# Performance work log

Hardware: AMD Instinct MI355X
Metric: run time of the kernel (lower is better)

The kernel has to match this reference:

```python
import math
import jax, jax.numpy as jnp
import numpy as np

HEADS = 16


def setup_inputs() -> dict:
    key = jax.random.key(0)
    k1, k2, k3, k4, k5 = jax.random.split(key, 5)
    B, S, D = 2, 2048, 1024
    return {
        "x": jax.random.normal(k1, (B, S, D), dtype=jnp.float32),
        "Wqkv": jax.random.normal(k2, (3 * D, D), dtype=jnp.float32) * (1.0 / math.sqrt(D)),
        "bqkv": jax.random.normal(k3, (3 * D,), dtype=jnp.float32) * 0.02,
        "Wo": jax.random.normal(k4, (D, D), dtype=jnp.float32) * (1.0 / math.sqrt(D)),
        "bo": jax.random.normal(k5, (D,), dtype=jnp.float32) * 0.02,
    }


def reference(x, Wqkv, bqkv, Wo, bo):
    B, S, D = x.shape
    H = HEADS
    hd = D // H  # head dim
    qkv = x @ Wqkv.T + bqkv                      # (B, S, 3D)
    # Faithful to torch: direct contiguous reshape (NOT a transpose-based head split)
    qkv = qkv.reshape(B, H, S, 3 * hd)           # (B, H, S, 3*hd)
    q, k, v = jnp.split(qkv, 3, axis=-1)         # each (B, H, S, hd)
    scores = jnp.einsum("bhsd,bhtd->bhst", q, k) * (1.0 / math.sqrt(hd))
    attn = jax.nn.softmax(scores, axis=-1)       # (B, H, S, S)
    vals = jnp.einsum("bhst,bhtd->bhsd", attn, v)
    vals = vals.reshape(B, S, D)                 # faithful direct reshape back
    return vals @ Wo.T + bo
```

## Files before the change

### kernel.cpp

```cpp
#include <hip/hip_runtime.h>
#include <stdint.h>

typedef unsigned short u16;
typedef __attribute__((ext_vector_type(8))) short short8;
typedef __attribute__((ext_vector_type(4))) float f32x4;
typedef __attribute__((ext_vector_type(16))) float f32x16;
typedef __attribute__((ext_vector_type(8))) __bf16 bf16x8;
typedef __attribute__((ext_vector_type(4))) unsigned u32x4;

#define DEV static __device__ __forceinline__

template <typename T>
DEV auto mfma_try(T a, T b, f32x4 c, int)
    -> decltype(__builtin_amdgcn_mfma_f32_16x16x32_bf16(a, b, c, 0, 0, 0)) {
  return __builtin_amdgcn_mfma_f32_16x16x32_bf16(a, b, c, 0, 0, 0);
}
template <typename T>
DEV f32x4 mfma_try(T a, T b, f32x4 c, long) {
  return __builtin_amdgcn_mfma_f32_16x16x32_bf16(
      __builtin_bit_cast(bf16x8, a), __builtin_bit_cast(bf16x8, b), c, 0, 0, 0);
}
DEV f32x4 MFMA(short8 a, short8 b, f32x4 c) { return mfma_try(a, b, c, 0); }

template <typename T>
DEV auto mfma32_try(T a, T b, f32x16 c, int)
    -> decltype(__builtin_amdgcn_mfma_f32_32x32x16_bf16(a, b, c, 0, 0, 0)) {
  return __builtin_amdgcn_mfma_f32_32x32x16_bf16(a, b, c, 0, 0, 0);
}
template <typename T>
DEV f32x16 mfma32_try(T a, T b, f32x16 c, long) {
  return __builtin_amdgcn_mfma_f32_32x32x16_bf16(
      __builtin_bit_cast(bf16x8, a), __builtin_bit_cast(bf16x8, b), c, 0, 0, 0);
}
DEV f32x16 MFMA32(short8 a, short8 b, f32x16 c) { return mfma32_try(a, b, c, 0); }

DEV void gload16(const u16* g, u16* lds) {
  __builtin_amdgcn_global_load_lds((unsigned int*)g, (unsigned int*)lds, 16, 0, 0);
}

DEV u16 f2bf(float f) {
  unsigned u = __float_as_uint(f);
  u = (u + 0x7FFFu + ((u >> 16) & 1u)) >> 16;
  return (u16)u;
}

DEV float exp2fast(float x) {
  float r;
  asm("v_exp_f32 %0, %1" : "=v"(r) : "v"(x));
  return r;
}

DEV unsigned cvtpk_bf16(float lo, float hi_) {
  unsigned r;
  asm("v_cvt_pk_bf16_f32 %0, %1, %2" : "=v"(r) : "v"(lo), "v"(hi_));
  return r;
}

DEV void permswap(unsigned& a, unsigned& b) {
  asm volatile("v_permlane32_swap_b32 %0, %1" : "+v"(a), "+v"(b));
}

__global__ void cvt_kernel(const float* __restrict__ x, const float* __restrict__ wq,
                           const float* __restrict__ wo, u16* __restrict__ xb,
                           u16* __restrict__ wqb, u16* __restrict__ wob) {
  const int N1 = 4194304 / 4, N2 = 3145728 / 4, N3 = 1048576 / 4;
  const int total = N1 + N2 + N3;
  for (int i = blockIdx.x * blockDim.x + threadIdx.x; i < total;
       i += gridDim.x * blockDim.x) {
    const float4* s;
    u16* d;
    int off;
    if (i < N1) { s = (const float4*)x; d = xb; off = i; }
    else if (i < N1 + N2) { s = (const float4*)wq; d = wqb; off = i - N1; }
    else { s = (const float4*)wo; d = wob; off = i - N1 - N2; }
    float4 v = s[off];
    ushort4 o;
    o.x = f2bf(v.x); o.y = f2bf(v.y); o.z = f2bf(v.z); o.w = f2bf(v.w);
    ((ushort4*)d)[off] = o;
  }
}

__global__ __launch_bounds__(256, 4) void gemm1_128(
    const u16* __restrict__ A, const u16* __restrict__ Bm,
    const float* __restrict__ bias,
    u16* __restrict__ Qb, u16* __restrict__ Kb, u16* __restrict__ Vb) {
  __shared__ u16 SM[128 * 136];
  const int K = 1024;
  const int tid = threadIdx.x;
  const int lane = tid & 63;
  const int wave = tid >> 6;
  const int wr = wave >> 1, wc = wave & 1;
  const int l15 = lane & 15, l4 = lane >> 4;
  const int m0 = blockIdx.y * 128, n0 = blockIdx.x * 128;

  f32x4 acc[4][4] = {};

  const u16* ga = A + (size_t)(m0 + (tid >> 2)) * K + (tid & 3) * 8;
  const u16* gb = Bm + (size_t)(n0 + (tid >> 2)) * K + (tid & 3) * 8;
  const size_t rstep = (size_t)64 * K;

  auto stage = [&](int buf, int kt) {
    u16* la = SM + buf * 8192 + tid * 8;
    u16* lb = la + 4096;
    gload16(ga + kt, la);
    gload16(ga + kt + rstep, la + 2048);
    gload16(gb + kt, lb);
    gload16(gb + kt + rstep, lb + 2048);
  };

  stage(0, 0);
  for (int t = 0; t < 32; ++t) {
    const int cur = t & 1;
    if (t + 1 < 32) {
      stage(cur ^ 1, (t + 1) * 32);
      asm volatile("s_waitcnt vmcnt(4)" ::: "memory");
    } else {
      asm volatile("s_waitcnt vmcnt(0)" ::: "memory");
    }
    __builtin_amdgcn_s_barrier();

    const u16* As = SM + cur * 8192;
    const u16* Bs = As + 4096;
    short8 af[4], bfr[4];
#pragma unroll
    for (int i = 0; i < 4; ++i)
      af[i] = *(const short8*)(As + (wr * 64 + i * 16 + l15) * 32 + l4 * 8);
#pragma unroll
    for (int i = 0; i < 4; ++i)
      bfr[i] = *(const short8*)(Bs + (wc * 64 + i * 16 + l15) * 32 + l4 * 8);
    __builtin_amdgcn_s_setprio(1);
#pragma unroll
    for (int i = 0; i < 4; ++i)
#pragma unroll
      for (int j = 0; j < 4; ++j) acc[i][j] = MFMA(af[i], bfr[j], acc[i][j]);
    __builtin_amdgcn_s_setprio(0);
    __builtin_amdgcn_s_barrier();
  }

#pragma unroll
  for (int nj = 0; nj < 4; ++nj) {
    const int cl = wc * 64 + nj * 16 + l15;
    const float bv = bias[n0 + cl];
#pragma unroll
    for (int mi = 0; mi < 4; ++mi)
#pragma unroll
      for (int r = 0; r < 4; ++r) {
        const int ml = wr * 64 + mi * 16 + l4 * 4 + r;
        SM[ml * 136 + cl] = f2bf(acc[mi][nj][r] + bv);
      }
  }
  __syncthreads();

  const int ml = tid >> 1;
  const int h = tid & 1;
  const int m = m0 + ml;
  const int c0 = n0 + h * 64;
  const int chunk = c0 / 192;
  const int sel = (c0 - chunk * 192) >> 6;
  u16* const dst = (sel == 0) ? Qb : ((sel == 1) ? Kb : Vb);
  const int s = m & 2047;
  const int bh = (m >> 11) * 16 + (s >> 7);
  const int s2 = (s & 127) * 16 + chunk;
  u16* const drow = dst + ((size_t)bh * 2048 + s2) * 64;
  const u16* const srow = SM + ml * 136 + h * 64;
#pragma unroll
  for (int g = 0; g < 8; ++g)
    *(short8*)(drow + g * 8) = *(const short8*)(srow + g * 8);
}

__global__ __launch_bounds__(256, 4) void gemm2_64(
    const u16* __restrict__ A, const u16* __restrict__ Bm,
    const float* __restrict__ bias, float* __restrict__ Cf) {
  __shared__ u16 SM2[2 * 6144];
  const int K = 1024, N = 1024;
  const int tid = threadIdx.x;
  const int lane = tid & 63;
  const int wave = tid >> 6;
  const int l15 = lane & 15, l4 = lane >> 4;
  const int m0 = blockIdx.y * 64, n0 = blockIdx.x * 128;

  f32x4 acc[4][2] = {};

  const u16* ga = A + (size_t)(m0 + (tid >> 2)) * K + (tid & 3) * 8;
  const u16* gb = Bm + (size_t)(n0 + (tid >> 2)) * K + (tid & 3) * 8;
  const size_t rstep = (size_t)64 * K;

  auto stage = [&](int buf, int kt) {
    u16* la = SM2 + buf * 6144 + tid * 8;
    u16* lb = SM2 + buf * 6144 + 2048 + tid * 8;
    gload16(ga + kt, la);
    gload16(gb + kt, lb);
    gload16(gb + kt + rstep, lb + 2048);
  };

  stage(0, 0);
  for (int t = 0; t < 32; ++t) {
    const int cur = t & 1;
    if (t + 1 < 32) {
      stage(cur ^ 1, (t + 1) * 32);
      asm volatile("s_waitcnt vmcnt(3)" ::: "memory");
    } else {
      asm volatile("s_waitcnt vmcnt(0)" ::: "memory");
    }
    __builtin_amdgcn_s_barrier();

    const u16* As = SM2 + cur * 6144;
    const u16* Bs = As + 2048;
    short8 af[4], bfr[2];
#pragma unroll
    for (int i = 0; i < 4; ++i)
      af[i] = *(const short8*)(As + (i * 16 + l15) * 32 + l4 * 8);
#pragma unroll
    for (int j = 0; j < 2; ++j)
      bfr[j] = *(const short8*)(Bs + (wave * 32 + j * 16 + l15) * 32 + l4 * 8);
    __builtin_amdgcn_s_setprio(1);
#pragma unroll
    for (int i = 0; i < 4; ++i)
#pragma unroll
      for (int j = 0; j < 2; ++j) acc[i][j] = MFMA(af[i], bfr[j], acc[i][j]);
    __builtin_amdgcn_s_setprio(0);
    __builtin_amdgcn_s_barrier();
  }

#pragma unroll
  for (int nj = 0; nj < 2; ++nj) {
    const int c = n0 + wave * 32 + nj * 16 + l15;
    const float bv = bias[c];
#pragma unroll
    for (int mi = 0; mi < 4; ++mi)
#pragma unroll
      for (int r = 0; r < 4; ++r) {
        const int m = m0 + mi * 16 + l4 * 4 + r;
        Cf[(size_t)m * N + c] = acc[mi][nj][r] + bv;
      }
  }
}

__global__ __launch_bounds__(256) void vtrans_kernel(const u16* __restrict__ Vn,
                                                     u16* __restrict__ VT) {
  __shared__ u16 T[64 * 72];
  const int tid = threadIdx.x;
  const int bh = blockIdx.x >> 5;
  const int s0 = (blockIdx.x & 31) * 64;
  const int r = tid >> 3, c8 = tid & 7;
#pragma unroll
  for (int i = 0; i < 2; ++i) {
    const int s = r + i * 32;
    short8 v = *(const short8*)(Vn + ((size_t)bh * 2048 + s0 + s) * 64 + c8 * 8);
#pragma unroll
    for (int j = 0; j < 8; ++j) T[(c8 * 8 + j) * 72 + s] = (u16)v[j];
  }
  __syncthreads();
#pragma unroll
  for (int i = 0; i < 2; ++i) {
    const int d = (tid >> 3) + i * 32;
    short8 v = *(const short8*)(&T[d * 72 + (tid & 7) * 8]);
    *(short8*)(VT + ((size_t)bh * 64 + d) * 2048 + s0 + (tid & 7) * 8) = v;
  }
}

__global__ __launch_bounds__(512) void attn_kernel(
    const u16* __restrict__ Qg, const u16* __restrict__ Kg,
    const u16* __restrict__ VTg, u16* __restrict__ v2) {
  __shared__ __align__(16) char smem[65536];
  u16* const KS = (u16*)smem;
  u16* const VS = (u16*)smem + 16384;
  float* const FM = (float*)smem;

  const int tid = threadIdx.x;
  const int lane = tid & 63;
  const int half = tid >> 8;
  const int tid256 = tid & 255;
  const int w4 = (tid >> 6) & 3;
  const int l31 = lane & 31;
  const int hi = lane >> 5;

  const int bid = blockIdx.x;
  const int logical = (bid & 7) * 64 + (bid >> 3);
  const int bh = logical >> 4;
  const int qt = logical & 15;

  const u16* Qh = Qg + (size_t)bh * 2048 * 64;
  const u16* Kh = Kg + (size_t)bh * 2048 * 64;
  const u16* VTh = VTg + (size_t)bh * 64 * 2048;

  const int q0 = qt * 128 + w4 * 32;
  const float C1 = 0.18033688f;

  short8 qf[4];
#pragma unroll
  for (int d_ = 0; d_ < 4; ++d_)
    qf[d_] = *(const short8*)(Qh + (size_t)(q0 + l31) * 64 + d_ * 16 + hi * 8);

  f32x16 ot[2] = {};
  float ls4[4] = {0.f, 0.f, 0.f, 0.f};

  const int r8 = tid256 >> 3;
  const int c16 = tid256 & 7;
  const int xr = l31 & 7;
  const int Tbase = half * 16;

  auto stage = [&](int buf, int T) {
    u16* kd = KS + (half * 2 + buf) * 4096 + tid256 * 8;
    u16* vd = VS + (half * 2 + buf) * 4096 + tid256 * 8;
#pragma unroll
    for (int i = 0; i < 2; ++i) {
      const int row = i * 32 + r8;
      gload16(Kh + (size_t)(T * 64 + row) * 64 + ((c16 ^ (row & 7)) * 8),
              kd + i * 2048);
    }
#pragma unroll
    for (int i = 0; i < 2; ++i) {
      const int d = i * 32 + r8;
      gload16(VTh + (size_t)d * 2048 + T * 64 + ((c16 ^ (d & 7)) * 8),
              vd + i * 2048);
    }
  };

  stage(0, Tbase);
  __syncthreads();

  for (int t = 0; t < 16; ++t) {
    const int cur = t & 1;
    if (t + 1 < 16) stage(cur ^ 1, Tbase + t + 1);

    const u16* Kb = KS + (half * 2 + cur) * 4096;
    const u16* Vb = VS + (half * 2 + cur) * 4096;

    f32x16 st[2] = {};
    __builtin_amdgcn_s_setprio(1);
#pragma unroll
    for (int n = 0; n < 2; ++n)
#pragma unroll
      for (int d_ = 0; d_ < 4; ++d_) {
        short8 kf = *(const short8*)(Kb + (n * 32 + l31) * 64 +
                                     (((d_ * 2 + hi) ^ xr) * 8));
        st[n] = MFMA32(kf, qf[d_], st[n]);
      }
    __builtin_amdgcn_s_setprio(0);

#pragma unroll
    for (int r = 0; r < 16; ++r) {
      st[0][r] = exp2fast(st[0][r] * C1);
      st[1][r] = exp2fast(st[1][r] * C1);
    }
#pragma unroll
    for (int i = 0; i < 4; ++i)
      ls4[i] += ((st[0][i] + st[0][i + 4]) + (st[0][i + 8] + st[0][i + 12])) +
                ((st[1][i] + st[1][i + 4]) + (st[1][i + 8] + st[1][i + 12]));

    short8 pf[2][2];
#pragma unroll
    for (int n = 0; n < 2; ++n) {
      unsigned W[4][2];
#pragma unroll
      for (int j = 0; j < 4; ++j)
#pragma unroll
        for (int pp = 0; pp < 2; ++pp)
          W[j][pp] = cvtpk_bf16(st[n][4 * j + 2 * pp], st[n][4 * j + 2 * pp + 1]);
#pragma unroll
      for (int ks = 0; ks < 2; ++ks) {
        unsigned x0 = W[2 * ks][0], y0 = W[2 * ks + 1][0];
        unsigned x1 = W[2 * ks][1], y1 = W[2 * ks + 1][1];
        permswap(x0, y0);
        permswap(x1, y1);
        u32x4 pw = {x0, x1, y0, y1};
        pf[n][ks] = __builtin_bit_cast(short8, pw);
      }
    }

    __builtin_amdgcn_s_setprio(1);
#pragma unroll
    for (int db = 0; db < 2; ++db)
#pragma unroll
      for (int ksg = 0; ksg < 4; ++ksg) {
        short8 vf = *(const short8*)(Vb + (db * 32 + l31) * 64 +
                                     (((ksg * 2 + hi) ^ xr) * 8));
        ot[db] = MFMA32(vf, pf[ksg >> 1][ksg & 1], ot[db]);
      }
    __builtin_amdgcn_s_setprio(0);

    __syncthreads();
  }

  float l = (ls4[0] + ls4[1]) + (ls4[2] + ls4[3]);
  l += __shfl_xor(l, 32);

  if (half == 1) {
    float* F = FM + (size_t)(w4 * 64 + lane) * 33;
#pragma unroll
    for (int r = 0; r < 16; ++r) {
      F[r] = ot[0][r];
      F[16 + r] = ot[1][r];
    }
    F[32] = l;
  }
  __syncthreads();
  if (half == 0) {
    const float* F = FM + (size_t)(w4 * 64 + lane) * 33;
    const float inv = 1.0f / (l + F[32]);

    const int s2v = q0 + l31;
    const int rowO = (bh >> 4) * 2048 + (bh & 15) * 128 + (s2v >> 4);
    const int colb = (s2v & 15) * 64;
#pragma unroll
    for (int db = 0; db < 2; ++db)
#pragma unroll
      for (int g = 0; g < 4; ++g) {
        ushort4 w;
        w.x = f2bf((ot[db][4 * g + 0] + F[db * 16 + 4 * g + 0]) * inv);
        w.y = f2bf((ot[db][4 * g + 1] + F[db * 16 + 4 * g + 1]) * inv);
        w.z = f2bf((ot[db][4 * g + 2] + F[db * 16 + 4 * g + 2]) * inv);
        w.w = f2bf((ot[db][4 * g + 3] + F[db * 16 + 4 * g + 3]) * inv);
        const int d = db * 32 + 8 * g + 4 * hi;
        *(ushort4*)(v2 + (size_t)rowO * 1024 + colb + d) = w;
      }
  }
}

extern "C" void kernel_launch(void* const* d_in, const int* in_sizes, int n_in,
                              void* d_out, int out_size, void* d_ws, size_t ws_size,
                              hipStream_t stream) {
  const float* x = (const float*)d_in[0];
  const float* Wqkv = (const float*)d_in[1];
  const float* bqkv = (const float*)d_in[2];
  const float* Wo = (const float*)d_in[3];
  const float* bo = (const float*)d_in[4];
  float* out = (float*)d_out;

  char* ws = (char*)d_ws;
  u16* xb   = (u16*)(ws);
  u16* wqb  = (u16*)(ws + 8388608);
  u16* wob  = (u16*)(ws + 14680064);
  u16* Qb   = (u16*)(ws + 16777216);
  u16* Kb   = (u16*)(ws + 25165824);
  u16* VTb  = (u16*)(ws + 33554432);
  u16* v2   = (u16*)(ws + 41943040);
  u16* Vnat = v2;

  cvt_kernel<<<2048, 256, 0, stream>>>(x, Wqkv, Wo, xb, wqb, wob);

  dim3 g1(24, 32);
  gemm1_128<<<g1, 256, 0, stream>>>(xb, wqb, bqkv, Qb, Kb, Vnat);

  vtrans_kernel<<<1024, 256, 0, stream>>>(Vnat, VTb);

  attn_kernel<<<512, 512, 0, stream>>>(Qb, Kb, VTb, v2);

  dim3 g2(8, 64);
  gemm2_64<<<g2, 256, 0, stream>>>(v2, wob, bo, out);
}
```

Before: 114.6 us.

## Triple-buffer QKV GEMM loads and give each attention wave two query tiles

The QKV projection GEMM moves from double to triple buffering in shared memory, keeping two K-tiles in flight, and drops the occupancy hint in its launch bounds. The attention kernel shrinks from 512 to 256 threads per block. Each wave now handles 64 query rows (two 32-row subtiles), so every K and V fragment read from LDS feeds two MFMAs. This aims to cut LDS traffic per MFMA and hide global load latency better, at the cost of more registers per wave and fewer waves per block to hide latency.

Result: slower. 130.4 us (+13.8%).

```diff
diff --git a/kernel.cpp b/kernel.cpp
--- a/kernel.cpp
+++ b/kernel.cpp
@@ -80,11 +80,11 @@
   }
 }
 
-__global__ __launch_bounds__(256, 4) void gemm1_128(
+__global__ __launch_bounds__(256) void gemm1_128(
     const u16* __restrict__ A, const u16* __restrict__ Bm,
     const float* __restrict__ bias,
     u16* __restrict__ Qb, u16* __restrict__ Kb, u16* __restrict__ Vb) {
-  __shared__ u16 SM[128 * 136];
+  __shared__ u16 SM[3 * 8192];
   const int K = 1024;
   const int tid = threadIdx.x;
   const int lane = tid & 63;
@@ -109,10 +109,13 @@
   };
 
   stage(0, 0);
+  stage(1, 32);
   for (int t = 0; t < 32; ++t) {
-    const int cur = t & 1;
-    if (t + 1 < 32) {
-      stage(cur ^ 1, (t + 1) * 32);
+    const int cur = t % 3;
+    if (t + 2 < 32) {
+      stage((t + 2) % 3, (t + 2) * 32);
+      asm volatile("s_waitcnt vmcnt(8)" ::: "memory");
+    } else if (t + 1 < 32) {
       asm volatile("s_waitcnt vmcnt(4)" ::: "memory");
     } else {
       asm volatile("s_waitcnt vmcnt(0)" ::: "memory");
@@ -259,7 +262,7 @@
   }
 }
 
-__global__ __launch_bounds__(512) void attn_kernel(
+__global__ __launch_bounds__(256) void attn_kernel(
     const u16* __restrict__ Qg, const u16* __restrict__ Kg,
     const u16* __restrict__ VTg, u16* __restrict__ v2) {
   __shared__ __align__(16) char smem[65536];
@@ -269,9 +272,9 @@
 
   const int tid = threadIdx.x;
   const int lane = tid & 63;
-  const int half = tid >> 8;
-  const int tid256 = tid & 255;
-  const int w4 = (tid >> 6) & 3;
+  const int wave = tid >> 6;
+  const int qw = wave & 1;
+  const int half = wave >> 1;
   const int l31 = lane & 31;
   const int hi = lane >> 5;
 
@@ -284,88 +287,96 @@
   const u16* Kh = Kg + (size_t)bh * 2048 * 64;
   const u16* VTh = VTg + (size_t)bh * 64 * 2048;
 
-  const int q0 = qt * 128 + w4 * 32;
+  const int q0 = qt * 128 + qw * 64;
   const float C1 = 0.18033688f;
 
-  short8 qf[4];
-#pragma unroll
-  for (int d_ = 0; d_ < 4; ++d_)
-    qf[d_] = *(const short8*)(Qh + (size_t)(q0 + l31) * 64 + d_ * 16 + hi * 8);
-
-  f32x16 ot[2] = {};
-  float ls4[4] = {0.f, 0.f, 0.f, 0.f};
-
-  const int r8 = tid256 >> 3;
-  const int c16 = tid256 & 7;
+  short8 qf[2][4];
+#pragma unroll
+  for (int qs = 0; qs < 2; ++qs)
+#pragma unroll
+    for (int d_ = 0; d_ < 4; ++d_)
+      qf[qs][d_] = *(const short8*)(Qh + (size_t)(q0 + qs * 32 + l31) * 64 +
+                                    d_ * 16 + hi * 8);
+
+  f32x16 ot[2][2] = {};
+  float ls4[2][4] = {};
+
   const int xr = l31 & 7;
-  const int Tbase = half * 16;
-
-  auto stage = [&](int buf, int T) {
-    u16* kd = KS + (half * 2 + buf) * 4096 + tid256 * 8;
-    u16* vd = VS + (half * 2 + buf) * 4096 + tid256 * 8;
-#pragma unroll
-    for (int i = 0; i < 2; ++i) {
-      const int row = i * 32 + r8;
-      gload16(Kh + (size_t)(T * 64 + row) * 64 + ((c16 ^ (row & 7)) * 8),
-              kd + i * 2048);
-    }
-#pragma unroll
-    for (int i = 0; i < 2; ++i) {
-      const int d = i * 32 + r8;
-      gload16(VTh + (size_t)d * 2048 + T * 64 + ((c16 ^ (d & 7)) * 8),
-              vd + i * 2048);
+
+  auto stage = [&](int buf, int tl) {
+#pragma unroll
+    for (int i = 0; i < 4; ++i) {
+      const int FB = i * 256 + tid;
+      const int hh = FB >> 9;
+      const int b = FB & 511;
+      const int r = b >> 3, cb = b & 7;
+      gload16(Kh + (size_t)(hh * 1024 + tl * 64 + r) * 64 + ((cb ^ (r & 7)) * 8),
+              KS + hh * 8192 + buf * 4096 + b * 8);
+    }
+#pragma unroll
+    for (int i = 0; i < 4; ++i) {
+      const int FB = i * 256 + tid;
+      const int hh = FB >> 9;
+      const int b = FB & 511;
+      const int r = b >> 3, cb = b & 7;
+      gload16(VTh + (size_t)r * 2048 + hh * 1024 + tl * 64 + ((cb ^ (r & 7)) * 8),
+              VS + hh * 8192 + buf * 4096 + b * 8);
     }
   };
 
-  stage(0, Tbase);
+  stage(0, 0);
   __syncthreads();
 
   for (int t = 0; t < 16; ++t) {
     const int cur = t & 1;
-    if (t + 1 < 16) stage(cur ^ 1, Tbase + t + 1);
-
-    const u16* Kb = KS + (half * 2 + cur) * 4096;
-    const u16* Vb = VS + (half * 2 + cur) * 4096;
-
-    f32x16 st[2] = {};
-    __builtin_amdgcn_s_setprio(1);
-#pragma unroll
-    for (int n = 0; n < 2; ++n)
+    if (t + 1 < 16) stage(cur ^ 1, t + 1);
+
+    const u16* Kb = KS + half * 8192 + cur * 4096;
+    const u16* Vb = VS + half * 8192 + cur * 4096;
+
+    short8 pf[2][2][2];
+#pragma unroll
+    for (int n = 0; n < 2; ++n) {
+      f32x16 s0 = {}, s1 = {};
+      __builtin_amdgcn_s_setprio(1);
 #pragma unroll
       for (int d_ = 0; d_ < 4; ++d_) {
         short8 kf = *(const short8*)(Kb + (n * 32 + l31) * 64 +
                                      (((d_ * 2 + hi) ^ xr) * 8));
-        st[n] = MFMA32(kf, qf[d_], st[n]);
-      }
-    __builtin_amdgcn_s_setprio(0);
-
-#pragma unroll
-    for (int r = 0; r < 16; ++r) {
-      st[0][r] = exp2fast(st[0][r] * C1);
-      st[1][r] = exp2fast(st[1][r] * C1);
-    }
-#pragma unroll
-    for (int i = 0; i < 4; ++i)
-      ls4[i] += ((st[0][i] + st[0][i + 4]) + (st[0][i + 8] + st[0][i + 12])) +
-                ((st[1][i] + st[1][i + 4]) + (st[1][i + 8] + st[1][i + 12]));
-
-    short8 pf[2][2];
-#pragma unroll
-    for (int n = 0; n < 2; ++n) {
-      unsigned W[4][2];
-#pragma unroll
-      for (int j = 0; j < 4; ++j)
-#pragma unroll
-        for (int pp = 0; pp < 2; ++pp)
-          W[j][pp] = cvtpk_bf16(st[n][4 * j + 2 * pp], st[n][4 * j + 2 * pp + 1]);
-#pragma unroll
-      for (int ks = 0; ks < 2; ++ks) {
-        unsigned x0 = W[2 * ks][0], y0 = W[2 * ks + 1][0];
-        unsigned x1 = W[2 * ks][1], y1 = W[2 * ks + 1][1];
-        permswap(x0, y0);
-        permswap(x1, y1);
-        u32x4 pw = {x0, x1, y0, y1};
-        pf[n][ks] = __builtin_bit_cast(short8, pw);
+        s0 = MFMA32(kf, qf[0][d_], s0);
+        s1 = MFMA32(kf, qf[1][d_], s1);
+      }
+      __builtin_amdgcn_s_setprio(0);
+
+#pragma unroll
+      for (int r = 0; r < 16; ++r) {
+        s0[r] = exp2fast(s0[r] * C1);
+        s1[r] = exp2fast(s1[r] * C1);
+      }
+#pragma unroll
+      for (int i = 0; i < 4; ++i) {
+        ls4[0][i] += (s0[i] + s0[i + 4]) + (s0[i + 8] + s0[i + 12]);
+        ls4[1][i] += (s1[i] + s1[i + 4]) + (s1[i + 8] + s1[i + 12]);
+      }
+
+#pragma unroll
+      for (int qs = 0; qs < 2; ++qs) {
+        const f32x16 p = qs ? s1 : s0;
+        unsigned W[4][2];
+#pragma unroll
+        for (int j = 0; j < 4; ++j)
+#pragma unroll
+          for (int pp = 0; pp < 2; ++pp)
+            W[j][pp] = cvtpk_bf16(p[4 * j + 2 * pp], p[4 * j + 2 * pp + 1]);
+#pragma unroll
+        for (int ks = 0; ks < 2; ++ks) {
+          unsigned x0 = W[2 * ks][0], y0 = W[2 * ks + 1][0];
+          unsigned x1 = W[2 * ks][1], y1 = W[2 * ks + 1][1];
+          permswap(x0, y0);
+          permswap(x1, y1);
+          u32x4 pw = {x0, x1, y0, y1};
+          pf[n][qs][ks] = __builtin_bit_cast(short8, pw);
+        }
       }
     }
 
@@ -376,45 +387,56 @@
       for (int ksg = 0; ksg < 4; ++ksg) {
         short8 vf = *(const short8*)(Vb + (db * 32 + l31) * 64 +
                                      (((ksg * 2 + hi) ^ xr) * 8));
-        ot[db] = MFMA32(vf, pf[ksg >> 1][ksg & 1], ot[db]);
+        ot[0][db] = MFMA32(vf, pf[ksg >> 1][0][ksg & 1], ot[0][db]);
+        ot[1][db] = MFMA32(vf, pf[ksg >> 1][1][ksg & 1], ot[1][db]);
       }
     __builtin_amdgcn_s_setprio(0);
 
     __syncthreads();
   }
 
-  float l = (ls4[0] + ls4[1]) + (ls4[2] + ls4[3]);
-  l += __shfl_xor(l, 32);
+  float l[2];
+#pragma unroll
+  for (int qs = 0; qs < 2; ++qs) {
+    l[qs] = (ls4[qs][0] + ls4[qs][1]) + (ls4[qs][2] + ls4[qs][3]);
+    l[qs] += __shfl_xor(l[qs], 32);
+  }
 
   if (half == 1) {
-    float* F = FM + (size_t)(w4 * 64 + lane) * 33;
-#pragma unroll
-    for (int r = 0; r < 16; ++r) {
-      F[r] = ot[0][r];
-      F[16 + r] = ot[1][r];
-    }
-    F[32] = l;
+#pragma unroll
+    for (int qs = 0; qs < 2; ++qs) {
+      float* F = FM + (size_t)((qw * 2 + qs) * 64 + lane) * 33;
+#pragma unroll
+      for (int r = 0; r < 16; ++r) {
+        F[r] = ot[qs][0][r];
+        F[16 + r] = ot[qs][1][r];
+      }
+      F[32] = l[qs];
+    }
   }
   __syncthreads();
   if (half == 0) {
-    const float* F = FM + (size_t)(w4 * 64 + lane) * 33;
-    const float inv = 1.0f / (l + F[32]);
-
-    const int s2v = q0 + l31;
-    const int rowO = (bh >> 4) * 2048 + (bh & 15) * 128 + (s2v >> 4);
-    const int colb = (s2v & 15) * 64;
-#pragma unroll
-    for (int db = 0; db < 2; ++db)
-#pragma unroll
-      for (int g = 0; g < 4; ++g) {
-        ushort4 w;
-        w.x = f2bf((ot[db][4 * g + 0] + F[db * 16 + 4 * g + 0]) * inv);
-        w.y = f2bf((ot[db][4 * g + 1] + F[db * 16 + 4 * g + 1]) * inv);
-        w.z = f2bf((ot[db][4 * g + 2] + F[db * 16 + 4 * g + 2]) * inv);
-        w.w = f2bf((ot[db][4 * g + 3] + F[db * 16 + 4 * g + 3]) * inv);
-        const int d = db * 32 + 8 * g + 4 * hi;
-        *(ushort4*)(v2 + (size_t)rowO * 1024 + colb + d) = w;
-      }
+#pragma unroll
+    for (int qs = 0; qs < 2; ++qs) {
+      const float* F = FM + (size_t)((qw * 2 + qs) * 64 + lane) * 33;
+      const float inv = 1.0f / (l[qs] + F[32]);
+
+      const int s2v = q0 + qs * 32 + l31;
+      const int rowO = (bh >> 4) * 2048 + (bh & 15) * 128 + (s2v >> 4);
+      const int colb = (s2v & 15) * 64;
+#pragma unroll
+      for (int db = 0; db < 2; ++db)
+#pragma unroll
+        for (int g = 0; g < 4; ++g) {
+          ushort4 w;
+          w.x = f2bf((ot[qs][db][4 * g + 0] + F[db * 16 + 4 * g + 0]) * inv);
+          w.y = f2bf((ot[qs][db][4 * g + 1] + F[db * 16 + 4 * g + 1]) * inv);
+          w.z = f2bf((ot[qs][db][4 * g + 2] + F[db * 16 + 4 * g + 2]) * inv);
+          w.w = f2bf((ot[qs][db][4 * g + 3] + F[db * 16 + 4 * g + 3]) * inv);
+          const int d = db * 32 + 8 * g + 4 * hi;
+          *(ushort4*)(v2 + (size_t)rowO * 1024 + colb + d) = w;
+        }
+    }
   }
 }
 
@@ -445,7 +467,7 @@
 
   vtrans_kernel<<<1024, 256, 0, stream>>>(Vnat, VTb);
 
-  attn_kernel<<<512, 512, 0, stream>>>(Qb, Kb, VTb, v2);
+  attn_kernel<<<512, 256, 0, stream>>>(Qb, Kb, VTb, v2);
 
   dim3 g2(8, 64);
   gemm2_64<<<g2, 256, 0, stream>>>(v2, wob, bo, out);
```

## Enlarge QKV GEMM tile to 256x192 with swizzled LDS and staged prefetch

Applied to the files above, without the earlier changes.

Replaces the 128x128 QKV projection GEMM with a 256x192 tile run by 512-thread blocks, using a K-step of 64 and XOR-swizzled shared memory panels. Global loads for the next K-step are spread across four sub-steps, and block IDs are remapped for better L2 locality. The aim is more reuse per loaded byte and fewer LDS bank conflicts. In exchange the kernel uses 112KB of dynamic LDS, which cuts occupancy and leaves the grid at 256 blocks, roughly one wave across the CUs.

Result: faster. 111.3 us (-2.9%).

```diff
diff --git a/kernel.cpp b/kernel.cpp
--- a/kernel.cpp
+++ b/kernel.cpp
@@ -80,92 +80,112 @@
   }
 }
 
-__global__ __launch_bounds__(256, 4) void gemm1_128(
+__global__ __launch_bounds__(512, 2) void gemm1_256(
     const u16* __restrict__ A, const u16* __restrict__ Bm,
     const float* __restrict__ bias,
     u16* __restrict__ Qb, u16* __restrict__ Kb, u16* __restrict__ Vb) {
-  __shared__ u16 SM[128 * 136];
+  extern __shared__ __align__(16) u16 SM[];
   const int K = 1024;
   const int tid = threadIdx.x;
   const int lane = tid & 63;
   const int wave = tid >> 6;
-  const int wr = wave >> 1, wc = wave & 1;
+  const int wr = wave >> 2;
+  const int wc = wave & 3;
   const int l15 = lane & 15, l4 = lane >> 4;
-  const int m0 = blockIdx.y * 128, n0 = blockIdx.x * 128;
-
-  f32x4 acc[4][4] = {};
-
-  const u16* ga = A + (size_t)(m0 + (tid >> 2)) * K + (tid & 3) * 8;
-  const u16* gb = Bm + (size_t)(n0 + (tid >> 2)) * K + (tid & 3) * 8;
-  const size_t rstep = (size_t)64 * K;
-
-  auto stage = [&](int buf, int kt) {
-    u16* la = SM + buf * 8192 + tid * 8;
-    u16* lb = la + 4096;
-    gload16(ga + kt, la);
-    gload16(ga + kt + rstep, la + 2048);
-    gload16(gb + kt, lb);
-    gload16(gb + kt + rstep, lb + 2048);
+
+  const int bid = blockIdx.x;
+  const int wg = (bid & 7) * 32 + (bid >> 3);
+  const int by = wg >> 4, bx = wg & 15;
+  const int m0 = by * 256, n0 = bx * 192;
+
+  f32x4 acc[8][3] = {};
+
+  const int srr = tid >> 3, scb = tid & 7;
+  const int ssw = (scb ^ (srr & 7)) * 8;
+
+  auto panel = [&](int Tn, int q) {
+    const u16* src =
+        (q < 4) ? A + (size_t)(m0 + q * 64 + srr) * K + Tn * 64 + ssw
+                : Bm + (size_t)(n0 + (q - 4) * 64 + srr) * K + Tn * 64 + ssw;
+    gload16(src, SM + ((Tn & 1) * 7 + q) * 4096 + tid * 8);
   };
 
-  stage(0, 0);
-  for (int t = 0; t < 32; ++t) {
-    const int cur = t & 1;
-    if (t + 1 < 32) {
-      stage(cur ^ 1, (t + 1) * 32);
-      asm volatile("s_waitcnt vmcnt(4)" ::: "memory");
-    } else {
-      asm volatile("s_waitcnt vmcnt(0)" ::: "memory");
-    }
-    __builtin_amdgcn_s_barrier();
-
-    const u16* As = SM + cur * 8192;
-    const u16* Bs = As + 4096;
-    short8 af[4], bfr[4];
-#pragma unroll
-    for (int i = 0; i < 4; ++i)
-      af[i] = *(const short8*)(As + (wr * 64 + i * 16 + l15) * 32 + l4 * 8);
-#pragma unroll
-    for (int i = 0; i < 4; ++i)
-      bfr[i] = *(const short8*)(Bs + (wc * 64 + i * 16 + l15) * 32 + l4 * 8);
-    __builtin_amdgcn_s_setprio(1);
-#pragma unroll
-    for (int i = 0; i < 4; ++i)
-#pragma unroll
-      for (int j = 0; j < 4; ++j) acc[i][j] = MFMA(af[i], bfr[j], acc[i][j]);
-    __builtin_amdgcn_s_setprio(0);
-    __builtin_amdgcn_s_barrier();
-  }
-
-#pragma unroll
-  for (int nj = 0; nj < 4; ++nj) {
-    const int cl = wc * 64 + nj * 16 + l15;
+#pragma unroll
+  for (int q = 0; q < 7; ++q) panel(0, q);
+
+  for (int T = 0; T < 16; ++T) {
+    const int base = (T & 1) * 7;
+    short8 bf[3];
+#pragma unroll
+    for (int p = 0; p < 4; ++p) {
+      if (T + 1 < 16) {
+        if (p == 0) { panel(T + 1, 0); panel(T + 1, 2); }
+        else if (p == 1) { panel(T + 1, 1); panel(T + 1, 3); }
+        else if (p == 2) { panel(T + 1, 4); panel(T + 1, 5); }
+        else { panel(T + 1, 6); }
+      }
+      if (p == 0) {
+        if (T + 1 < 16) asm volatile("s_waitcnt vmcnt(2)" ::: "memory");
+        else asm volatile("s_waitcnt vmcnt(0)" ::: "memory");
+      }
+      __builtin_amdgcn_s_barrier();
+
+      const int g = p & 1, kk = p >> 1;
+      if (g == 0) {
+#pragma unroll
+        for (int nj = 0; nj < 3; ++nj) {
+          const int rb = wc * 48 + nj * 16 + l15;
+          const int qb = 4 + (rb >> 6), rrb = rb & 63;
+          bf[nj] = *(const short8*)(SM + (base + qb) * 4096 + rrb * 64 +
+                                    (((kk * 4 + l4) ^ (rrb & 7)) * 8));
+        }
+      }
+      short8 af[4];
+      const int qa = wr * 2 + g;
+#pragma unroll
+      for (int mi = 0; mi < 4; ++mi) {
+        const int rr = mi * 16 + l15;
+        af[mi] = *(const short8*)(SM + (base + qa) * 4096 + rr * 64 +
+                                  (((kk * 4 + l4) ^ (rr & 7)) * 8));
+      }
+      __builtin_amdgcn_s_setprio(1);
+#pragma unroll
+      for (int mi = 0; mi < 4; ++mi)
+#pragma unroll
+        for (int nj = 0; nj < 3; ++nj)
+          acc[g * 4 + mi][nj] = MFMA(af[mi], bf[nj], acc[g * 4 + mi][nj]);
+      __builtin_amdgcn_s_setprio(0);
+    }
+  }
+  __syncthreads();
+
+#pragma unroll
+  for (int nj = 0; nj < 3; ++nj) {
+    const int cl = wc * 48 + nj * 16 + l15;
     const float bv = bias[n0 + cl];
 #pragma unroll
-    for (int mi = 0; mi < 4; ++mi)
+    for (int mi = 0; mi < 8; ++mi)
 #pragma unroll
       for (int r = 0; r < 4; ++r) {
-        const int ml = wr * 64 + mi * 16 + l4 * 4 + r;
-        SM[ml * 136 + cl] = f2bf(acc[mi][nj][r] + bv);
+        const int ml = wr * 128 + mi * 16 + l4 * 4 + r;
+        SM[ml * 200 + cl] = f2bf(acc[mi][nj][r] + bv);
       }
   }
   __syncthreads();
 
-  const int ml = tid >> 1;
-  const int h = tid & 1;
-  const int m = m0 + ml;
-  const int c0 = n0 + h * 64;
-  const int chunk = c0 / 192;
-  const int sel = (c0 - chunk * 192) >> 6;
-  u16* const dst = (sel == 0) ? Qb : ((sel == 1) ? Kb : Vb);
-  const int s = m & 2047;
-  const int bh = (m >> 11) * 16 + (s >> 7);
-  const int s2 = (s & 127) * 16 + chunk;
-  u16* const drow = dst + ((size_t)bh * 2048 + s2) * 64;
-  const u16* const srow = SM + ml * 136 + h * 64;
-#pragma unroll
-  for (int g = 0; g < 8; ++g)
-    *(short8*)(drow + g * 8) = *(const short8*)(srow + g * 8);
+  for (int k = tid; k < 768; k += 512) {
+    const int ml = k & 255, h = k >> 8;
+    const int m = m0 + ml;
+    const int s = m & 2047;
+    const int bh = (m >> 11) * 16 + (s >> 7);
+    const int s2 = (s & 127) * 16 + bx;
+    u16* const dst = (h == 0) ? Qb : ((h == 1) ? Kb : Vb);
+    u16* const drow = dst + ((size_t)bh * 2048 + s2) * 64;
+    const u16* const srow = SM + ml * 200 + h * 64;
+#pragma unroll
+    for (int g2 = 0; g2 < 8; ++g2)
+      *(short8*)(drow + g2 * 8) = *(const short8*)(srow + g2 * 8);
+  }
 }
 
 __global__ __launch_bounds__(256, 4) void gemm2_64(
@@ -440,8 +460,9 @@
 
   cvt_kernel<<<2048, 256, 0, stream>>>(x, Wqkv, Wo, xb, wqb, wob);
 
-  dim3 g1(24, 32);
-  gemm1_128<<<g1, 256, 0, stream>>>(xb, wqb, bqkv, Qb, Kb, Vnat);
+  hipFuncSetAttribute((const void*)gemm1_256,
+                      hipFuncAttributeMaxDynamicSharedMemorySize, 114688);
+  gemm1_256<<<256, 512, 114688, stream>>>(xb, wqb, bqkv, Qb, Kb, Vnat);
 
   vtrans_kernel<<<1024, 256, 0, stream>>>(Vnat, VTb);
 
```
